# Performance work log

Measured on AMD Instinct MI355X. Metric: run time of the kernel, lower is better.

## Reference

```python
import jax, jax.numpy as jnp
import numpy as np

EPS = 1e-6


def _expand_mask(mask, D, H, W):
    # mask: (B,1,f,f,f) bool -> (B,1,D,H,W) via repeat_interleave on each spatial axis
    m = jnp.repeat(mask, D // mask.shape[2], axis=2)
    m = jnp.repeat(m, H // mask.shape[3], axis=3)
    m = jnp.repeat(m, W // mask.shape[4], axis=4)
    return m


def setup_inputs() -> dict:
    key = jax.random.key(0)
    ks = jax.random.split(key, 10)
    B, C, D, H, W = 2, 192, 32, 32, 32
    K, HID = 7, 4 * C
    x = jax.random.normal(ks[0], (B, C, D, H, W), dtype=jnp.float32)
    mask = jax.random.randint(ks[1], (B, 1, 8, 8, 8), 0, 2) > 0
    dw_w = jax.random.normal(ks[2], (C, 1, K, K, K), dtype=jnp.float32) * (1.0 / np.sqrt(K**3))
    dw_b = jnp.zeros((C,), dtype=jnp.float32)
    ln_w = jnp.ones((C,), dtype=jnp.float32)
    ln_b = jnp.zeros((C,), dtype=jnp.float32)
    w1 = jax.random.normal(ks[3], (C, HID), dtype=jnp.float32) * (1.0 / np.sqrt(C))
    b1 = jnp.zeros((HID,), dtype=jnp.float32)
    w2 = jax.random.normal(ks[4], (HID, C), dtype=jnp.float32) * (1.0 / np.sqrt(HID))
    b2 = jnp.zeros((C,), dtype=jnp.float32)
    gamma = jnp.full((C,), 1e-6, dtype=jnp.float32)
    return {"x": x, "mask": mask, "dw_w": dw_w, "dw_b": dw_b, "ln_w": ln_w,
            "ln_b": ln_b, "w1": w1, "b1": b1, "w2": w2, "b2": b2, "gamma": gamma}


def reference(x, mask, dw_w, dw_b, ln_w, ln_b, w1, b1, w2, b2, gamma):
    B, C, D, H, W = x.shape
    m = _expand_mask(mask, D, H, W)              # (B,1,D,H,W) bool
    mf = m.astype(x.dtype)

    # depthwise 3D conv, SAME padding (padding = kernel//2), groups = C
    y = jax.lax.conv_general_dilated(
        x, dw_w, window_strides=(1, 1, 1), padding='SAME',
        dimension_numbers=('NCDHW', 'OIDHW', 'NCDHW'),
        feature_group_count=C)
    y = y + dw_b[None, :, None, None, None]

    # channels_last: (B,D,H,W,C)
    y = jnp.transpose(y, (0, 2, 3, 4, 1))

    # sparse LayerNorm over channel dim: normalize all tokens, keep only active
    # (equivalent to gather->LN->scatter-into-zeros in the original)
    mu = jnp.mean(y, axis=-1, keepdims=True)
    var = jnp.mean(jnp.square(y - mu), axis=-1, keepdims=True)
    ln = (y - mu) * jax.lax.rsqrt(var + EPS) * ln_w + ln_b
    ln = ln * jnp.transpose(mf, (0, 2, 3, 4, 1))  # zero inactive tokens

    # pointwise MLP
    h = jax.nn.gelu(jnp.einsum('bdhwc,ce->bdhwe', ln, w1) + b1, approximate=False)
    o = jnp.einsum('bdhwe,ec->bdhwc', h, w2) + b2
    o = gamma * o

    # back to channels_first and final sparse mask
    o = jnp.transpose(o, (0, 4, 1, 2, 3)) * mf
    return o
```

## Files before the change

### kernel.cpp

```cpp
#include <hip/hip_runtime.h>
#include <hip/hip_bf16.h>

typedef __attribute__((ext_vector_type(2))) float f2v;
typedef __attribute__((ext_vector_type(4))) float f4v;
typedef __attribute__((ext_vector_type(8))) short bf8v;
typedef __attribute__((ext_vector_type(8))) _Float16 h8v;

#define NPOS 32768
#define CCH  192
#define HID  768

#define WS_Y    ((size_t)0)
#define WS_B1F  ((size_t)25165824)
#define WS_B2F  ((size_t)25460736)
#define WS_WPF  ((size_t)25755648)
#define WS_B3F  ((size_t)26056704)
#define WS_TOTAL_MFMA ((size_t)35690496)
#define WS_TOTAL_DOT2 ((size_t)26056704)

__device__ inline unsigned short f2bf(float f){
  unsigned int u = __float_as_uint(f);
  u += 0x7FFFu + ((u >> 16) & 1u);
  return (unsigned short)(u >> 16);
}
__device__ inline float bf2f(unsigned short s){
  return __uint_as_float(((unsigned int)s) << 16);
}
__device__ inline float gelu_f(float x){
  float u = 0.7978845608028654f * x * fmaf(0.044715f, x*x, 1.0f);
  float e = __expf(2.0f*u);
  float th = __fdividef(e - 1.0f, e + 1.0f);
  return 0.5f*x*(1.0f + th);
}

#define DOT2(A, X, W) \
  asm("v_dot2_f32_f16 %0, %1, %2, %0" : "+v"(A) : "v"(X), "s"(W))

__global__ __launch_bounds__(256) void compact_kernel(
    const int* __restrict__ mask, int* __restrict__ list)
{
  __shared__ unsigned short cnt[256];
  __shared__ int pref[257];
  int t = threadIdx.x;
  int m[4], c0 = 0;
  #pragma unroll
  for (int i = 0; i < 4; ++i) { m[i] = mask[t*4 + i]; c0 += (m[i] != 0); }
  cnt[t] = (unsigned short)c0;
  __syncthreads();
  if (t == 0) {
    int s = 0;
    for (int i = 0; i < 256; ++i) { pref[i] = s; s += cnt[i]; }
    pref[256] = s;
  }
  __syncthreads();
  int na = pref[256];
  int pa = pref[t];
  int pi = na + (t*4 - pref[t]);
  #pragma unroll
  for (int i = 0; i < 4; ++i) {
    if (m[i]) list[pa++] = t*4 + i;
    else      list[pi++] = t*4 + i;
  }
  if (t == 0) list[1024] = na;
}

#define ZSTR 712
__global__ __launch_bounds__(256) void conv_mfma_kernel(
    const float* __restrict__ x, const float* __restrict__ dw_b,
    const unsigned short* __restrict__ b3f, unsigned short* __restrict__ yc)
{
  __shared__ unsigned short tile[22*ZSTR];

  int bid = blockIdx.x;
  int c = bid % 192;
  int r = bid / 192;
  int xq = r & 1, yq = (r >> 1) & 1, zh = (r >> 2) & 1, b = r >> 3;
  int tx0 = xq*16, ty0 = yq*16, zb = zh*16;

  int tid = threadIdx.x;
  const float* xsrc = x + ((size_t)(b*CCH + c))*NPOS;

  #pragma unroll
  for (int it = 0; it < 8; ++it) {
    int idx = tid + 256*it;
    if (idx < 1936) {
      int ci = idx & 3;
      int row = idx >> 2;
      int lz = row / 22, ly = row - lz*22;
      int gz = zb - 3 + lz, gy = ty0 - 3 + ly;
      f4v v0 = {0.f,0.f,0.f,0.f}, v1 = {0.f,0.f,0.f,0.f};
      if (((unsigned)gz < 32u) & ((unsigned)gy < 32u) & (ci < 3)) {
        int gx0 = tx0 - 4 + 8*ci;
        const float* src = xsrc + (size_t)gz*1024 + gy*32;
        if ((unsigned)gx0 <= 28u)     v0 = *(const f4v*)(src + gx0);
        if ((unsigned)(gx0+4) <= 28u) v1 = *(const f4v*)(src + gx0 + 4);
      }
      h8v pk;
      pk[0] = (_Float16)v0[0]; pk[1] = (_Float16)v0[1];
      pk[2] = (_Float16)v0[2]; pk[3] = (_Float16)v0[3];
      pk[4] = (_Float16)v1[0]; pk[5] = (_Float16)v1[1];
      pk[6] = (_Float16)v1[2]; pk[7] = (_Float16)v1[3];
      *(h8v*)(tile + lz*ZSTR + ly*32 + ci*8) = pk;
    }
  }
  __syncthreads();

  int wv = tid >> 6, lane = tid & 63;
  int q = lane >> 4, zm = lane & 15;

  const unsigned short* abase = tile + (size_t)zm*ZSTR + q*8;
  const unsigned short* bbase = b3f + ((size_t)c*49)*512 + (size_t)lane*8;

  f4v acc[4];
  #pragma unroll
  for (int t = 0; t < 4; ++t) acc[t] = (f4v){0.f,0.f,0.f,0.f};

  #pragma unroll 1
  for (int kz = 0; kz < 7; ++kz) {
    h8v Bt[7];
    #pragma unroll
    for (int ky = 0; ky < 7; ++ky)
      Bt[ky] = *(const h8v*)(bbase + (size_t)(kz*7 + ky)*512);
    h8v Af[10];
    #pragma unroll
    for (int rr = 0; rr < 10; ++rr)
      Af[rr] = *(const h8v*)(abase + kz*ZSTR + (4*wv + rr)*32);
    #pragma unroll
    for (int ky = 0; ky < 7; ++ky) {
      acc[0] = __builtin_amdgcn_mfma_f32_16x16x32_f16(Af[ky+0], Bt[ky], acc[0], 0, 0, 0);
      acc[1] = __builtin_amdgcn_mfma_f32_16x16x32_f16(Af[ky+1], Bt[ky], acc[1], 0, 0, 0);
      acc[2] = __builtin_amdgcn_mfma_f32_16x16x32_f16(Af[ky+2], Bt[ky], acc[2], 0, 0, 0);
      acc[3] = __builtin_amdgcn_mfma_f32_16x16x32_f16(Af[ky+3], Bt[ky], acc[3], 0, 0, 0);
    }
  }

  float bias = dw_b[c];
  int cz = zh*4 + q;
  int cx = (tx0 >> 2) + (zm >> 2);
  int xr = zm & 3;
  int cy = (ty0 >> 2) + wv;
  int cell = cz*64 + cy*8 + cx;
  unsigned short* yb0 = yc + (((size_t)(b*512 + cell))*192 + c)*64 + xr;
  #pragma unroll
  for (int t = 0; t < 4; ++t) {
    unsigned short* yb = yb0 + t*4;
    yb[0]  = f2bf(acc[t][0] + bias);
    yb[16] = f2bf(acc[t][1] + bias);
    yb[32] = f2bf(acc[t][2] + bias);
    yb[48] = f2bf(acc[t][3] + bias);
  }
}

__global__ __launch_bounds__(256, 6) void conv_dw_f16_kernel(
    const float* __restrict__ x, const float* __restrict__ dw_b,
    const unsigned int* __restrict__ wpf, unsigned short* __restrict__ yc)
{
  __shared__ unsigned short ring[22*528];

  int bid = blockIdx.x;
  int c = bid % 192;
  int r = bid / 192;
  int xq = r & 1, yq = (r >> 1) & 1, zh = (r >> 2) & 1, b = r >> 3;
  int tx0 = xq*16, ty0 = yq*16, zb = zh*16;

  int tid = threadIdx.x;
  const float* xsrc = x + ((size_t)(b*CCH + c))*NPOS;

  for (int idx = tid; idx < 2904; idx += 256) {
    int sl = idx / 132;
    int rem = idx - sl*132;
    int rr = rem / 6, ci = rem - rr*6;
    int zi = zb - 3 + sl, gy = ty0 - 3 + rr, gx = tx0 - 4 + 4*ci;
    f4v v = {0.f, 0.f, 0.f, 0.f};
    if ((unsigned)zi < 32u && (unsigned)gy < 32u && (unsigned)gx <= 28u)
      v = *(const f4v*)(xsrc + (size_t)zi*1024 + gy*32 + gx);
    union { _Float16 h[4]; uint2 u2; } pk;
    pk.h[0] = (_Float16)v[0]; pk.h[1] = (_Float16)v[1];
    pk.h[2] = (_Float16)v[2]; pk.h[3] = (_Float16)v[3];
    *(uint2*)(ring + sl*528 + rr*24 + ci*4) = pk.u2;
  }
  __syncthreads();

  int p = tid & 15, zl = tid >> 4;
  int px = p & 3, py = p >> 2;
  int y0 = py*4, px4 = px*4;
  const unsigned short* base = ring + zl*528 + y0*24 + px4;
  const unsigned int* wb = wpf + (size_t)c*392;

  float acc[4][4];
  #pragma unroll
  for (int i = 0; i < 4; ++i)
    #pragma unroll
    for (int j = 0; j < 4; ++j) acc[i][j] = 0.f;

  #pragma unroll 1
  for (int s = 0; s < 7; ++s) {
    const unsigned short* sb = base + s*528;
    const unsigned int* wrow = wb + s*56;
    #pragma unroll
    for (int rr = 0; rr < 10; ++rr) {
      const unsigned short* rb = sb + rr*24;
      uint2 q0 = *(const uint2*)(rb);
      uint2 q1 = *(const uint2*)(rb + 4);
      uint2 q2 = *(const uint2*)(rb + 8);
      unsigned int D[6] = {q0.x, q0.y, q1.x, q1.y, q2.x, q2.y};
      #pragma unroll
      for (int dy = 0; dy < 4; ++dy) {
        int ky = rr - dy;
        if (ky < 0 || ky > 6) continue;
        const unsigned int* wk = wrow + ky*8;
        #pragma unroll
        for (int t = 0; t < 4; ++t) {
          DOT2(acc[dy][0], D[t],   wk[t]);
          DOT2(acc[dy][1], D[t+1], wk[4+t]);
          DOT2(acc[dy][2], D[t+1], wk[t]);
          DOT2(acc[dy][3], D[t+2], wk[4+t]);
        }
      }
    }
  }

  float bias = dw_b[c];
  int z = zb + zl;
  int cz = z >> 2, cx = (tx0 >> 2) + px, cy = (ty0 >> 2) + py;
  int cell = cz*64 + cy*8 + cx;
  unsigned short* ybase = yc + (((size_t)(b*512 + cell))*192 + c)*64;
  int tokz = (z & 3)*16;
  #pragma unroll
  for (int dy = 0; dy < 4; ++dy) {
    ushort4 o;
    o.x = f2bf(acc[dy][0] + bias);
    o.y = f2bf(acc[dy][1] + bias);
    o.z = f2bf(acc[dy][2] + bias);
    o.w = f2bf(acc[dy][3] + bias);
    *(ushort4*)(ybase + tokz + dy*4) = o;
  }
}

__global__ __launch_bounds__(256) void conv_dw_f32_kernel(
    const float* __restrict__ x, const float* __restrict__ dw_w,
    const float* __restrict__ dw_b, unsigned short* __restrict__ yc)
{
  __shared__ float ring[22*528];

  int bid = blockIdx.x;
  int c = bid % 192;
  int r = bid / 192;
  int xq = r & 1, yq = (r >> 1) & 1, zh = (r >> 2) & 1, b = r >> 3;
  int tx0 = xq*16, ty0 = yq*16, zb = zh*16;

  int tid = threadIdx.x;
  const float* xsrc = x + ((size_t)(b*CCH + c))*NPOS;

  for (int idx = tid; idx < 2904; idx += 256) {
    int sl = idx / 132;
    int rem = idx - sl*132;
    int rr = rem / 6, ci = rem - rr*6;
    int zi = zb - 3 + sl, gy = ty0 - 3 + rr, gx = tx0 - 4 + 4*ci;
    f4v v = {0.f, 0.f, 0.f, 0.f};
    if ((unsigned)zi < 32u && (unsigned)gy < 32u && (unsigned)gx <= 28u)
      v = *(const f4v*)(xsrc + (size_t)zi*1024 + gy*32 + gx);
    *(f4v*)(ring + sl*528 + rr*24 + ci*4) = v;
  }
  __syncthreads();

  int p = tid & 15, zl = tid >> 4;
  int px = p & 3, py = p >> 2;
  int y0 = py*4, px4 = px*4;
  const float* base = ring + zl*528 + y0*24 + px4;
  const float* wbase = dw_w + (size_t)c*343;

  f2v acc[8];
  #pragma unroll
  for (int i = 0; i < 8; ++i) acc[i] = (f2v){0.f, 0.f};

  #pragma unroll 1
  for (int s = 0; s < 7; ++s) {
    const float* sb = base + s*528;
    f4v n0 = *(const f4v*)(sb);
    f4v n1 = *(const f4v*)(sb + 4);
    f4v n2 = *(const f4v*)(sb + 8);
    #pragma unroll
    for (int rr = 0; rr < 10; ++rr) {
      f4v r0 = n0, r1 = n1, r2 = n2;
      if (rr < 9) {
        n0 = *(const f4v*)(sb + (rr+1)*24);
        n1 = *(const f4v*)(sb + (rr+1)*24 + 4);
        n2 = *(const f4v*)(sb + (rr+1)*24 + 8);
      }
      f2v pr[10];
      pr[1] = (f2v){r0[1], r0[2]};
      pr[2] = (f2v){r0[2], r0[3]};
      pr[3] = (f2v){r0[3], r1[0]};
      pr[4] = (f2v){r1[0], r1[1]};
      pr[5] = (f2v){r1[1], r1[2]};
      pr[6] = (f2v){r1[2], r1[3]};
      pr[7] = (f2v){r1[3], r2[0]};
      pr[8] = (f2v){r2[0], r2[1]};
      pr[9] = (f2v){r2[1], r2[2]};
      #pragma unroll
      for (int dy = 0; dy < 4; ++dy) {
        int ky = rr - dy;
        if (ky < 0 || ky > 6) continue;
        #pragma unroll
        for (int kx = 0; kx < 7; ++kx) {
          float w = wbase[s*49 + ky*7 + kx];
          f2v wv = (f2v){w, w};
          acc[dy*2+0] = __builtin_elementwise_fma(wv, pr[kx+1], acc[dy*2+0]);
          acc[dy*2+1] = __builtin_elementwise_fma(wv, pr[kx+3], acc[dy*2+1]);
        }
      }
    }
  }

  float bias = dw_b[c];
  int z = zb + zl;
  int cz = z >> 2, cx = (tx0 >> 2) + px, cy = (ty0 >> 2) + py;
  int cell = cz*64 + cy*8 + cx;
  unsigned short* ybase = yc + (((size_t)(b*512 + cell))*192 + c)*64;
  int tokz = (z & 3)*16;
  #pragma unroll
  for (int dy = 0; dy < 4; ++dy) {
    ushort4 o;
    o.x = f2bf(acc[dy*2+0][0] + bias);
    o.y = f2bf(acc[dy*2+0][1] + bias);
    o.z = f2bf(acc[dy*2+1][0] + bias);
    o.w = f2bf(acc[dy*2+1][1] + bias);
    *(ushort4*)(ybase + tokz + dy*4) = o;
  }
}

__global__ __launch_bounds__(256) void prep_w_kernel(
    const float* __restrict__ w1, const float* __restrict__ w2,
    const float* __restrict__ dw_w,
    unsigned short* __restrict__ b1f, unsigned short* __restrict__ b2f,
    unsigned int* __restrict__ wpf, unsigned short* __restrict__ b3f)
{
  int gid = blockIdx.x*256 + threadIdx.x;
  if (gid < 18432) {
    int fi = gid;
    int lane = fi & 63, fr = fi >> 6;
    int nt = fr / 6, ks = fr - nt*6;
    int n  = nt*16 + (lane & 15);
    int kb = ks*32 + (lane >> 4)*8;
    #pragma unroll
    for (int j = 0; j < 8; ++j) b1f[fi*8 + j] = f2bf(w1[(kb+j)*HID + n]);
  } else if (gid < 36864) {
    int fi = gid - 18432;
    int lane = fi & 63, fr = fi >> 6;
    int nt = fr / 24, ks = fr - nt*24;
    int n  = nt*16 + (lane & 15);
    int kb = ks*32 + (lane >> 4)*8;
    #pragma unroll
    for (int j = 0; j < 8; ++j) b2f[fi*8 + j] = f2bf(w2[(kb+j)*CCH + n]);
  } else if (gid < 46272) {
    int ci = gid - 36864;
    int cch = ci / 49, t7 = ci - cch*49;
    const float* wr = dw_w + cch*343 + t7*7;
    float w[8];
    #pragma unroll
    for (int j = 0; j < 7; ++j) w[j] = wr[j];
    w[7] = 0.f;
    union { _Float16 h[2]; unsigned int u; } pk;
    #pragma unroll
    for (int t = 0; t < 4; ++t) {
      pk.h[0] = (t == 0) ? (_Float16)0.f : (_Float16)w[2*t-1];
      pk.h[1] = (_Float16)w[2*t];
      wpf[ci*8 + t] = pk.u;
    }
    #pragma unroll
    for (int t = 0; t < 4; ++t) {
      pk.h[0] = (_Float16)w[2*t];
      pk.h[1] = (_Float16)w[2*t+1];
      wpf[ci*8 + 4 + t] = pk.u;
    }
  } else if (gid < 648384) {
    int fi = gid - 46272;
    int lane = fi & 63, frag = fi >> 6;
    int cch = frag / 49, tap = frag - cch*49;
    const float* wr = dw_w + cch*343 + tap*7;
    int q = lane >> 4, n = lane & 15;
    h8v pk;
    #pragma unroll
    for (int j = 0; j < 8; ++j) {
      int t = q*8 + j - n - 1;
      pk[j] = (t >= 0 && t <= 6) ? (_Float16)wr[t] : (_Float16)0.f;
    }
    *(h8v*)(b3f + (size_t)fi*8) = pk;
  }
}

template<int COMPACT>
__global__ __launch_bounds__(256) void mlp_kernel(
    const unsigned short* __restrict__ yc, const unsigned short* __restrict__ b1f,
    const unsigned short* __restrict__ b2f, const float* __restrict__ b1,
    const float* __restrict__ b2, const float* __restrict__ gamma,
    const float* __restrict__ ln_w, const float* __restrict__ ln_b,
    const int* __restrict__ mask, const int* __restrict__ list,
    float* __restrict__ out)
{
  int bid = blockIdx.x;
  int cid, active;
  if constexpr (COMPACT) {
    int na = list[1024];
    cid = list[bid];
    active = bid < na;
  } else {
    cid = bid;
    active = (mask[bid] != 0);
  }
  int b = cid >> 9, cell = cid & 511;
  int cz = cell >> 6, cy = (cell >> 3) & 7, cx = cell & 7;
  int z0 = cz*4, y0 = cy*4, x0 = cx*4;
  int tid = threadIdx.x, wave = tid >> 6, lane = tid & 63;
  int lq = lane >> 4, ln15 = lane & 15;

  if (!active) {
    f4v z4 = {0.f, 0.f, 0.f, 0.f};
    #pragma unroll
    for (int pp = 0; pp < 12; ++pp) {
      int i4 = tid + 256*pp;
      int c = i4 >> 4, rem = i4 & 15;
      int dz = rem >> 2, dy = rem & 3;
      *(f4v*)(out + ((size_t)(b*CCH + c))*NPOS
                  + (size_t)(z0+dz)*1024 + (y0+dy)*32 + x0) = z4;
    }
    return;
  }

  __shared__ __align__(16) char uni[26112];
  unsigned short* ymat = (unsigned short*)uni;
  unsigned short* hbuf = (unsigned short*)uni;
  __shared__ unsigned short aFrag[12288];
  __shared__ float sred[2][4][64];
  __shared__ float murs[2][64];

  const unsigned short* ysrc = yc + (size_t)cid*12288;

  #pragma unroll
  for (int k = 0; k < 12; ++k) {
    int idx = tid + 256*k;
    int c = idx >> 4, t4 = idx & 15;
    *(ushort4*)(ymat + c*68 + t4*4) = *(const ushort4*)(ysrc + c*64 + t4*4);
  }
  __syncthreads();

  {
    int tok = tid & 63, part = tid >> 6;
    float S = 0.f, Q = 0.f;
    #pragma unroll
    for (int j = 0; j < 48; ++j) {
      float v = bf2f(ymat[(part*48 + j)*68 + tok]);
      S += v; Q = fmaf(v, v, Q);
    }
    sred[0][part][tok] = S; sred[1][part][tok] = Q;
  }
  __syncthreads();
  if (tid < 64) {
    float S = sred[0][0][tid] + sred[0][1][tid] + sred[0][2][tid] + sred[0][3][tid];
    float Q = sred[1][0][tid] + sred[1][1][tid] + sred[1][2][tid] + sred[1][3][tid];
    float m = S*(1.f/192.f);
    float var = Q*(1.f/192.f) - m*m;
    murs[0][tid] = m;
    murs[1][tid] = rsqrtf(var + 1e-6f);
  }
  __syncthreads();

  #pragma unroll
  for (int k = 0; k < 6; ++k) {
    int fi = tid + 256*k;
    int lane2 = fi & 63, rest = fi >> 6;
    int mt = rest / 6, ks = rest - mt*6;
    int tok = mt*16 + (lane2 & 15);
    int cc0 = ks*32 + (lane2 >> 4)*8;
    float m = murs[0][tok], rs = murs[1][tok];
    f4v lw0 = *(const f4v*)(ln_w + cc0), lw1 = *(const f4v*)(ln_w + cc0 + 4);
    f4v lb0 = *(const f4v*)(ln_b + cc0), lb1 = *(const f4v*)(ln_b + cc0 + 4);
    union { bf8v v; unsigned short u[8]; } pk;
    #pragma unroll
    for (int j = 0; j < 4; ++j) {
      float v0 = (bf2f(ymat[(cc0+j)*68 + tok])   - m)*rs*lw0[j] + lb0[j];
      float v1 = (bf2f(ymat[(cc0+4+j)*68 + tok]) - m)*rs*lw1[j] + lb1[j];
      pk.u[j] = f2bf(v0); pk.u[4+j] = f2bf(v1);
    }
    *(bf8v*)(aFrag + fi*8) = pk.v;
  }
  __syncthreads();

  f4v acc2[4][3];
  #pragma unroll
  for (int mt = 0; mt < 4; ++mt)
    #pragma unroll
    for (int nt = 0; nt < 3; ++nt)
      acc2[mt][nt] = (f4v){0.f, 0.f, 0.f, 0.f};

  const unsigned short* p1base = b1f + wave*2*3072 + lane*8;
  const unsigned short* p2base = b2f + wave*3*12288 + lane*8;

  bf8v B1r[12];
  #pragma unroll
  for (int i = 0; i < 12; ++i) {
    int jj = i / 6, ks = i - jj*6;
    B1r[i] = *(const bf8v*)(p1base + jj*3072 + ks*512);
  }

  #pragma unroll 1
  for (int ch = 0; ch < 6; ++ch) {
    bf8v B2r[12];
    const unsigned short* p2 = p2base + ch*2048;
    #pragma unroll
    for (int ks2 = 0; ks2 < 4; ++ks2)
      #pragma unroll
      for (int nt = 0; nt < 3; ++nt)
        B2r[ks2*3 + nt] = *(const bf8v*)(p2 + nt*12288 + ks2*512);

    f4v a1[2][4];
    #pragma unroll
    for (int jj = 0; jj < 2; ++jj)
      #pragma unroll
      for (int mt = 0; mt < 4; ++mt) a1[jj][mt] = (f4v){0.f,0.f,0.f,0.f};
    #pragma unroll
    for (int ks = 0; ks < 6; ++ks) {
      bf8v Af[4];
      #pragma unroll
      for (int mt = 0; mt < 4; ++mt)
        Af[mt] = *(const bf8v*)(aFrag + ((mt*6 + ks)*64 + lane)*8);
      #pragma unroll
      for (int jj = 0; jj < 2; ++jj)
        #pragma unroll
        for (int mt = 0; mt < 4; ++mt)
          a1[jj][mt] = __builtin_amdgcn_mfma_f32_16x16x32_bf16(Af[mt], B1r[jj*6+ks], a1[jj][mt], 0, 0, 0);
    }

    if (ch < 5) {
      const unsigned short* p1 = p1base + (ch+1)*24576;
      #pragma unroll
      for (int i = 0; i < 12; ++i) {
        int jj = i / 6, ks = i - jj*6;
        B1r[i] = *(const bf8v*)(p1 + jj*3072 + ks*512);
      }
    }

    #pragma unroll
    for (int jj = 0; jj < 2; ++jj) {
      float b1v = b1[(ch*8 + wave*2 + jj)*16 + ln15];
      int lane_hi = jj*2 + (ln15 >> 3);
      #pragma unroll
      for (int mt = 0; mt < 4; ++mt)
        #pragma unroll
        for (int rr = 0; rr < 4; ++rr) {
          float g = gelu_f(a1[jj][mt][rr] + b1v);
          int elem = ((mt*4 + wave)*64 + lane_hi*16 + (lq*4 + rr))*8 + (lane & 7);
          hbuf[elem] = f2bf(g);
        }
    }
    __syncthreads();
    #pragma unroll
    for (int ks2 = 0; ks2 < 4; ++ks2) {
      bf8v A2[4];
      #pragma unroll
      for (int mt = 0; mt < 4; ++mt)
        A2[mt] = *(const bf8v*)(hbuf + ((mt*4 + ks2)*64 + lane)*8);
      #pragma unroll
      for (int nt = 0; nt < 3; ++nt)
        #pragma unroll
        for (int mt = 0; mt < 4; ++mt)
          acc2[mt][nt] = __builtin_amdgcn_mfma_f32_16x16x32_bf16(A2[mt], B2r[ks2*3+nt], acc2[mt][nt], 0, 0, 0);
    }
    __syncthreads();
  }

  #pragma unroll
  for (int nt = 0; nt < 3; ++nt) {
    int c = (wave*3 + nt)*16 + ln15;
    float gm = gamma[c], bb = b2[c];
    size_t cbase = ((size_t)(b*CCH + c))*NPOS + (size_t)(y0 + lq)*32 + x0;
    #pragma unroll
    for (int mt = 0; mt < 4; ++mt) {
      f4v o;
      o[0] = gm*(acc2[mt][nt][0] + bb);
      o[1] = gm*(acc2[mt][nt][1] + bb);
      o[2] = gm*(acc2[mt][nt][2] + bb);
      o[3] = gm*(acc2[mt][nt][3] + bb);
      *(f4v*)(out + cbase + (size_t)(z0 + mt)*1024) = o;
    }
  }
}

extern "C" void kernel_launch(void* const* d_in, const int* in_sizes, int n_in,
                              void* d_out, int out_size, void* d_ws, size_t ws_size,
                              hipStream_t stream) {
  const float* x     = (const float*)d_in[0];
  const int*   mask  = (const int*)  d_in[1];
  const float* dw_w  = (const float*)d_in[2];
  const float* dw_b  = (const float*)d_in[3];
  const float* ln_w  = (const float*)d_in[4];
  const float* ln_b  = (const float*)d_in[5];
  const float* w1    = (const float*)d_in[6];
  const float* b1    = (const float*)d_in[7];
  const float* w2    = (const float*)d_in[8];
  const float* b2    = (const float*)d_in[9];
  const float* gamma = (const float*)d_in[10];
  float* out = (float*)d_out;
  char* ws = (char*)d_ws;

  unsigned short* yc  = (unsigned short*)(ws + WS_Y);
  unsigned short* b1f = (unsigned short*)(ws + WS_B1F);
  unsigned short* b2f = (unsigned short*)(ws + WS_B2F);
  unsigned int*   wpf = (unsigned int*)(ws + WS_WPF);
  unsigned short* b3f = (unsigned short*)(ws + WS_B3F);
  int*            lst = (int*)(ws + WS_WPF);

  bool mfma_ok = ws_size >= WS_TOTAL_MFMA;
  bool dot2_ok = ws_size >= WS_TOTAL_DOT2;
  int prep_grid = mfma_ok ? 2533 : (dot2_ok ? 181 : 144);
  prep_w_kernel<<<prep_grid, 256, 0, stream>>>(w1, w2, dw_w, b1f, b2f, wpf, b3f);
  if (mfma_ok) {
    compact_kernel<<<1, 256, 0, stream>>>(mask, lst);
    conv_mfma_kernel<<<3072, 256, 0, stream>>>(x, dw_b, b3f, yc);
    mlp_kernel<1><<<1024, 256, 0, stream>>>(yc, b1f, b2f, b1, b2, gamma, ln_w, ln_b, mask, lst, out);
  } else if (dot2_ok) {
    conv_dw_f16_kernel<<<3072, 256, 0, stream>>>(x, dw_b, wpf, yc);
    mlp_kernel<0><<<1024, 256, 0, stream>>>(yc, b1f, b2f, b1, b2, gamma, ln_w, ln_b, mask, nullptr, out);
  } else {
    conv_dw_f32_kernel<<<3072, 256, 0, stream>>>(x, dw_w, dw_b, yc);
    mlp_kernel<0><<<1024, 256, 0, stream>>>(yc, b1f, b2f, b1, b2, gamma, ln_w, ln_b, mask, nullptr, out);
  }
}
```

Baseline: 227.0 us.

## Split MLP work by token tile per wave and pass hidden activations via bpermute

The fused MLP is restructured so that each wave owns one 16-token tile and computes all hidden and output channels for it, instead of splitting channels across waves. The first GEMM is computed transposed (weights as A operand), so the GELU output can be rearranged into the second GEMM's A-fragment layout with ds_bpermute lane shuffles. This removes the shared-memory hidden buffer and the two block barriers per chunk. In exchange, every wave now streams all W1/W2 fragments from global/L2 with no register prefetch, which multiplies weight-load traffic by four per block.

```diff
diff --git a/kernel.cpp b/kernel.cpp
--- a/kernel.cpp
+++ b/kernel.cpp
@@ -428,9 +428,7 @@
     return;
   }
 
-  __shared__ __align__(16) char uni[26112];
-  unsigned short* ymat = (unsigned short*)uni;
-  unsigned short* hbuf = (unsigned short*)uni;
+  __shared__ __align__(16) unsigned short ymat[192*68];
   __shared__ unsigned short aFrag[12288];
   __shared__ float sred[2][4][64];
   __shared__ float murs[2][64];
@@ -487,103 +485,76 @@
   }
   __syncthreads();
 
-  f4v acc2[4][3];
-  #pragma unroll
-  for (int mt = 0; mt < 4; ++mt)
-    #pragma unroll
-    for (int nt = 0; nt < 3; ++nt)
-      acc2[mt][nt] = (f4v){0.f, 0.f, 0.f, 0.f};
-
-  const unsigned short* p1base = b1f + wave*2*3072 + lane*8;
-  const unsigned short* p2base = b2f + wave*3*12288 + lane*8;
-
-  bf8v B1r[12];
-  #pragma unroll
-  for (int i = 0; i < 12; ++i) {
-    int jj = i / 6, ks = i - jj*6;
-    B1r[i] = *(const bf8v*)(p1base + jj*3072 + ks*512);
-  }
+  f4v acc[12];
+  #pragma unroll
+  for (int nt = 0; nt < 12; ++nt) acc[nt] = (f4v){0.f,0.f,0.f,0.f};
+
+  int addrA = ((((lq & 1)*2)*16 + ln15) << 2);
+  int addrB = addrA + 64;
+  bool hiq = lq >= 2;
 
   #pragma unroll 1
   for (int ch = 0; ch < 6; ++ch) {
-    bf8v B2r[12];
-    const unsigned short* p2 = p2base + ch*2048;
-    #pragma unroll
-    for (int ks2 = 0; ks2 < 4; ++ks2)
+    f4v D[8];
+    #pragma unroll
+    for (int j2 = 0; j2 < 8; ++j2) D[j2] = (f4v){0.f,0.f,0.f,0.f};
+    #pragma unroll
+    for (int ks = 0; ks < 6; ++ks) {
+      bf8v Afk = *(const bf8v*)(aFrag + ((wave*6 + ks)*64 + lane)*8);
+      const unsigned short* b1p = b1f + ((size_t)(ch*8)*6 + ks)*512 + lane*8;
       #pragma unroll
-      for (int nt = 0; nt < 3; ++nt)
-        B2r[ks2*3 + nt] = *(const bf8v*)(p2 + nt*12288 + ks2*512);
-
-    f4v a1[2][4];
-    #pragma unroll
-    for (int jj = 0; jj < 2; ++jj)
+      for (int j2 = 0; j2 < 8; ++j2) {
+        bf8v B1 = *(const bf8v*)(b1p + (size_t)j2*6*512);
+        D[j2] = __builtin_amdgcn_mfma_f32_16x16x32_bf16(B1, Afk, D[j2], 0, 0, 0);
+      }
+    }
+    unsigned int p0[8], p1[8];
+    #pragma unroll
+    for (int j2 = 0; j2 < 8; ++j2) {
+      f4v bb = *(const f4v*)(b1 + (ch*8 + j2)*16 + lq*4);
+      float g0 = gelu_f(D[j2][0] + bb[0]);
+      float g1 = gelu_f(D[j2][1] + bb[1]);
+      float g2 = gelu_f(D[j2][2] + bb[2]);
+      float g3 = gelu_f(D[j2][3] + bb[3]);
+      p0[j2] = (unsigned int)f2bf(g0) | ((unsigned int)f2bf(g1) << 16);
+      p1[j2] = (unsigned int)f2bf(g2) | ((unsigned int)f2bf(g3) << 16);
+    }
+    #pragma unroll
+    for (int k2 = 0; k2 < 4; ++k2) {
+      int e = k2*2, o = k2*2 + 1;
+      unsigned int v0a = (unsigned int)__builtin_amdgcn_ds_bpermute(addrA, (int)p0[e]);
+      unsigned int v0b = (unsigned int)__builtin_amdgcn_ds_bpermute(addrA, (int)p0[o]);
+      unsigned int v1a = (unsigned int)__builtin_amdgcn_ds_bpermute(addrA, (int)p1[e]);
+      unsigned int v1b = (unsigned int)__builtin_amdgcn_ds_bpermute(addrA, (int)p1[o]);
+      unsigned int v2a = (unsigned int)__builtin_amdgcn_ds_bpermute(addrB, (int)p0[e]);
+      unsigned int v2b = (unsigned int)__builtin_amdgcn_ds_bpermute(addrB, (int)p0[o]);
+      unsigned int v3a = (unsigned int)__builtin_amdgcn_ds_bpermute(addrB, (int)p1[e]);
+      unsigned int v3b = (unsigned int)__builtin_amdgcn_ds_bpermute(addrB, (int)p1[o]);
+      union { unsigned int u[4]; bf8v v; } A2;
+      A2.u[0] = hiq ? v0b : v0a;
+      A2.u[1] = hiq ? v1b : v1a;
+      A2.u[2] = hiq ? v2b : v2a;
+      A2.u[3] = hiq ? v3b : v3a;
+      const unsigned short* b2p = b2f + ((size_t)(ch*4 + k2))*512 + lane*8;
       #pragma unroll
-      for (int mt = 0; mt < 4; ++mt) a1[jj][mt] = (f4v){0.f,0.f,0.f,0.f};
-    #pragma unroll
-    for (int ks = 0; ks < 6; ++ks) {
-      bf8v Af[4];
-      #pragma unroll
-      for (int mt = 0; mt < 4; ++mt)
-        Af[mt] = *(const bf8v*)(aFrag + ((mt*6 + ks)*64 + lane)*8);
-      #pragma unroll
-      for (int jj = 0; jj < 2; ++jj)
-        #pragma unroll
-        for (int mt = 0; mt < 4; ++mt)
-          a1[jj][mt] = __builtin_amdgcn_mfma_f32_16x16x32_bf16(Af[mt], B1r[jj*6+ks], a1[jj][mt], 0, 0, 0);
-    }
-
-    if (ch < 5) {
-      const unsigned short* p1 = p1base + (ch+1)*24576;
-      #pragma unroll
-      for (int i = 0; i < 12; ++i) {
-        int jj = i / 6, ks = i - jj*6;
-        B1r[i] = *(const bf8v*)(p1 + jj*3072 + ks*512);
+      for (int nt = 0; nt < 12; ++nt) {
+        bf8v B2 = *(const bf8v*)(b2p + (size_t)nt*24*512);
+        acc[nt] = __builtin_amdgcn_mfma_f32_16x16x32_bf16(A2.v, B2, acc[nt], 0, 0, 0);
       }
     }
-
-    #pragma unroll
-    for (int jj = 0; jj < 2; ++jj) {
-      float b1v = b1[(ch*8 + wave*2 + jj)*16 + ln15];
-      int lane_hi = jj*2 + (ln15 >> 3);
-      #pragma unroll
-      for (int mt = 0; mt < 4; ++mt)
-        #pragma unroll
-        for (int rr = 0; rr < 4; ++rr) {
-          float g = gelu_f(a1[jj][mt][rr] + b1v);
-          int elem = ((mt*4 + wave)*64 + lane_hi*16 + (lq*4 + rr))*8 + (lane & 7);
-          hbuf[elem] = f2bf(g);
-        }
-    }
-    __syncthreads();
-    #pragma unroll
-    for (int ks2 = 0; ks2 < 4; ++ks2) {
-      bf8v A2[4];
-      #pragma unroll
-      for (int mt = 0; mt < 4; ++mt)
-        A2[mt] = *(const bf8v*)(hbuf + ((mt*4 + ks2)*64 + lane)*8);
-      #pragma unroll
-      for (int nt = 0; nt < 3; ++nt)
-        #pragma unroll
-        for (int mt = 0; mt < 4; ++mt)
-          acc2[mt][nt] = __builtin_amdgcn_mfma_f32_16x16x32_bf16(A2[mt], B2r[ks2*3+nt], acc2[mt][nt], 0, 0, 0);
-    }
-    __syncthreads();
-  }
-
-  #pragma unroll
-  for (int nt = 0; nt < 3; ++nt) {
-    int c = (wave*3 + nt)*16 + ln15;
+  }
+
+  #pragma unroll
+  for (int nt = 0; nt < 12; ++nt) {
+    int c = nt*16 + ln15;
     float gm = gamma[c], bb = b2[c];
-    size_t cbase = ((size_t)(b*CCH + c))*NPOS + (size_t)(y0 + lq)*32 + x0;
-    #pragma unroll
-    for (int mt = 0; mt < 4; ++mt) {
-      f4v o;
-      o[0] = gm*(acc2[mt][nt][0] + bb);
-      o[1] = gm*(acc2[mt][nt][1] + bb);
-      o[2] = gm*(acc2[mt][nt][2] + bb);
-      o[3] = gm*(acc2[mt][nt][3] + bb);
-      *(f4v*)(out + cbase + (size_t)(z0 + mt)*1024) = o;
-    }
+    f4v o;
+    o[0] = gm*(acc[nt][0] + bb);
+    o[1] = gm*(acc[nt][1] + bb);
+    o[2] = gm*(acc[nt][2] + bb);
+    o[3] = gm*(acc[nt][3] + bb);
+    *(f4v*)(out + ((size_t)(b*CCH + c))*NPOS
+              + (size_t)(z0 + wave)*1024 + (y0 + lq)*32 + x0) = o;
   }
 }
 
```

After: 350.7 us. +54.5%, slower.
